# Kernel tuning notes

Measured on AMD Instinct MI355X. Metric: run time of the kernel, lower is better.

Reference implementation:

```python
import jax, jax.numpy as jnp
import numpy as np

B, C, D, L, H = 128, 1000, 300, 40, 100


def setup_inputs() -> dict:
    key = jax.random.key(0)
    ks = jax.random.split(key, 16)
    def rn(i, shape, sc=1.0):
        return (jax.random.normal(ks[i], shape, jnp.float32) * sc).astype(jnp.float32)
    return {
        "utt": rn(0, (B, L, D)),
        "sys_slots": rn(1, (B, D), 0.1),
        "conf_slots": rn(2, (B, D), 0.1),
        "conf_values": rn(3, (B, D), 0.1),
        "y_past_state": jax.random.uniform(ks[4], (B, C), jnp.float32),
        "slot_emb": rn(5, (C, D), 0.1),
        "value_emb": rn(6, (C, D), 0.1),
        "Wc": rn(7, (D, 2 * D), 0.05), "bc": jnp.zeros((D,), jnp.float32),
        "conv_w1": rn(8, (D, D, 1), 0.05), "conv_b1": jnp.zeros((D,), jnp.float32),
        "conv_w2": rn(9, (D, D, 2), 0.05), "conv_b2": jnp.zeros((D,), jnp.float32),
        "conv_w3": rn(10, (D, D, 3), 0.05), "conv_b3": jnp.zeros((D,), jnp.float32),
        "Wd": rn(11, (H, D), 0.05), "bd": jnp.zeros((H,), jnp.float32),
        "Wmr": rn(12, (H, D), 0.05), "bmr": jnp.zeros((H,), jnp.float32),
        "Wmc": rn(13, (H, D), 0.05), "bmc": jnp.zeros((H,), jnp.float32),
        "Wj": rn(14, (1, H), 0.05), "bj": jnp.zeros((1,), jnp.float32),
    }


def _conv_relu_pool(x_ncl, w, b):
    # x_ncl: [B, D, L]; w: [F, D, k] -> relu(conv) then global max-pool over time -> [B, F]
    y = jax.lax.conv_general_dilated(x_ncl, w, (1,), 'VALID',
                                     dimension_numbers=('NCH', 'OIH', 'NCH'))
    y = jax.nn.relu(y + b[None, :, None])
    return jnp.max(y, axis=2)


def _sig_linear(x, W, b):
    # Sequential(Sigmoid, Linear): Linear applied to sigmoid(x)
    return jax.nn.sigmoid(x) @ W.T + b


def reference(utt, sys_slots, conf_slots, conf_values, y_past_state,
              slot_emb, value_emb, Wc, bc,
              conv_w1, conv_b1, conv_w2, conv_b2, conv_w3, conv_b3,
              Wd, bd, Wmr, bmr, Wmc, bmc, Wj, bj):
    # CNN utterance encoder: sum of 3 conv branches (filter widths 1,2,3)
    x = jnp.transpose(utt, (0, 2, 1))  # [B, D, L]
    final_utt = (_conv_relu_pool(x, conv_w1, conv_b1)
                 + _conv_relu_pool(x, conv_w2, conv_b2)
                 + _conv_relu_pool(x, conv_w3, conv_b3))  # [B, D]

    # candidates_transform = sigmoid(Linear(cat(slot_emb, value_emb)))
    cand = jax.nn.sigmoid(jnp.concatenate([slot_emb, value_emb], axis=1) @ Wc.T + bc)  # [C, D]

    # fused version of the per-batch repeat/addcmul loop: [B, C, D]
    contrib = cand[None, :, :] * final_utt[:, None, :]

    y1 = _sig_linear(_sig_linear(contrib, Wd, bd), Wj, bj)  # [B, C, 1]

    # system-act request gate: ([C,D]@[D,B]) @ [B,D] -> [C, D]
    m_r = (slot_emb @ sys_slots.T) @ final_utt
    y2 = _sig_linear(_sig_linear(m_r, Wmr, bmr), Wj, bj)  # [C, 1]

    # system-act confirm gate
    m_c = ((slot_emb @ conf_slots.T) * (value_emb @ conf_values.T)) @ final_utt  # [C, D]
    y3 = _sig_linear(_sig_linear(m_c, Wmc, bmc), Wj, bj)  # [C, 1]

    y_presoftmax = y1 + y2[None, :, :] + y3[None, :, :]  # [B, C, 1]
    combine = 0.5
    return combine * y_presoftmax[..., 0] + (1.0 - combine) * y_past_state  # [B, C]
```

## Files before the change

kernel.cpp:

```cpp
#include <hip/hip_runtime.h>
#include <hip/hip_bf16.h>

#define OFF_SYST    0
#define OFF_CONFST  153600
#define OFF_CONFVT  307200
#define OFF_WMRT    460800
#define OFF_WMCT    580800
#define OFF_FU      700800
#define OFF_Y23     854400
#define OFF_BDP     858432
#define OFF_WJP     858880
#define OFF_BCP     859392
#define OFF_XBF     860672
#define OFF_WALLT   4137472
#define OFF_PBF     5366272
#define OFF_FUBF    25027072
#define OFF_CATSV   25108992
#define OFF_WCPK    26419712
#define OFF_CANDBF  26829312
#define OFF_WDFRAG  27484672

typedef short bf16x8_t __attribute__((ext_vector_type(8)));
typedef float f32x4_t  __attribute__((ext_vector_type(4)));

__device__ __forceinline__ float sigmoidf_fast(float x) {
    return __builtin_amdgcn_rcpf(1.0f + __expf(-x));
}
__device__ __forceinline__ unsigned short f2bf(float x) {
    unsigned int u = __float_as_uint(x);
    unsigned int r = (u + 0x7FFFu + ((u >> 16) & 1u)) >> 16;
    return (unsigned short)r;
}
__device__ __forceinline__ float bf2f(unsigned short h) {
    return __uint_as_float(((unsigned int)h) << 16);
}

__global__ void pack_kernel(const float* __restrict__ w1, const float* __restrict__ w2,
                            const float* __restrict__ w3, const float* __restrict__ Wc,
                            const float* __restrict__ Wd, const float* __restrict__ Wmr,
                            const float* __restrict__ Wmc, const float* __restrict__ sys,
                            const float* __restrict__ confs, const float* __restrict__ confv,
                            const float* __restrict__ bd, const float* __restrict__ Wj,
                            const float* __restrict__ bc, const float* __restrict__ slot,
                            const float* __restrict__ value,
                            unsigned short* __restrict__ WallTbf,
                            unsigned short* __restrict__ WdFrag,
                            float* __restrict__ bdPad, float* __restrict__ WjPad,
                            float* __restrict__ bcPad,
                            float* __restrict__ sysT, float* __restrict__ confsT,
                            float* __restrict__ confvT, float* __restrict__ WmrT,
                            float* __restrict__ WmcT,
                            unsigned short* __restrict__ catsv,
                            unsigned short* __restrict__ WcPk) {
    int idx = blockIdx.x * blockDim.x + threadIdx.x;
    if (idx < 614400) {
        int tap = idx / 102400;
        int rem = idx - tap * 102400;
        int f = rem / 320, k = rem % 320;
        float v = 0.0f;
        if (f < 300 && k < 300) {
            int fd = f * 300 + k;
            if (tap == 0)      v = w1[fd];
            else if (tap == 1) v = w2[fd * 2 + 0];
            else if (tap == 2) v = w2[fd * 2 + 1];
            else               v = w3[fd * 3 + (tap - 3)];
        }
        WallTbf[idx] = f2bf(v);
    } else if (idx < 650240) {
        int i = idx - 614400;
        int entry = i >> 3, e = i & 7;
        int kt = entry / 448;
        int r = entry - kt * 448;
        int ni = r >> 6, lane = r & 63;
        int j = ni * 16 + (lane & 15);
        int k = kt * 32 + (lane >> 4) * 8 + e;
        float v = (j < 100 && k < 300) ? Wd[j * 300 + k] : 0.0f;
        WdFrag[i] = f2bf(v);
    } else if (idx < 650352) {
        int j = idx - 650240;
        bdPad[j] = (j < 100) ? bd[j] : 0.0f;
    } else if (idx < 650464) {
        int j = idx - 650352;
        WjPad[j] = (j < 100) ? Wj[j] : 0.0f;
    } else if (idx < 650784) {
        int j = idx - 650464;
        bcPad[j] = (j < 300) ? bc[j] : 0.0f;
    } else if (idx < 765984) {
        int i = idx - 650784; int m = i / 38400; int r = i % 38400;
        int d = r / 128, b = r % 128;
        const float* src = (m == 0) ? sys : ((m == 1) ? confs : confv);
        float* dst = (m == 0) ? sysT : ((m == 1) ? confsT : confvT);
        dst[r] = src[b * 300 + d];
    } else if (idx < 795984) {
        int i = idx - 765984; int f = i / 100, j = i % 100;
        WmrT[i] = Wmr[j * 300 + f];
    } else if (idx < 825984) {
        int i = idx - 795984; int f = i / 100, j = i % 100;
        WmcT[i] = Wmc[j * 300 + f];
    } else if (idx < 1481344) {
        int i = idx - 825984;
        int c = i / 640, k = i % 640;
        float v = 0.0f;
        if (c < 1000) {
            if (k < 300)                   v = slot[c * 300 + k];
            else if (k >= 320 && k < 620)  v = value[c * 300 + (k - 320)];
        }
        catsv[i] = f2bf(v);
    } else if (idx < 1686144) {
        int i = idx - 1481344;
        int f = i / 640, k = i % 640;
        float v = 0.0f;
        if (f < 300) {
            if (k < 300)                   v = Wc[f * 600 + k];
            else if (k >= 320 && k < 620)  v = Wc[f * 600 + 300 + (k - 320)];
        }
        WcPk[i] = f2bf(v);
    }
}

__global__ void xcvt_kernel(const float* __restrict__ utt, unsigned short* __restrict__ Xbf) {
    int idx = blockIdx.x * blockDim.x + threadIdx.x;
    int m = idx / 320, k = idx % 320;
    float v = (k < 300) ? utt[m * 300 + k] : 0.0f;
    Xbf[idx] = f2bf(v);
}

__global__ __launch_bounds__(256, 2) void gemm1_kernel(const unsigned short* __restrict__ Xbf,
        const unsigned short* __restrict__ WallTbf, unsigned short* __restrict__ Pbf) {
    __shared__ __attribute__((aligned(16))) short As[128 * 40];
    __shared__ __attribute__((aligned(16))) short Bs[128 * 40];
    const int tid = threadIdx.x;
    const int m0 = blockIdx.x * 128;
    const int n0 = blockIdx.y * 128;
    const int lane = tid & 63;
    const int w = tid >> 6;
    const int wrow = w >> 1, wcol = w & 1;
    const int ln = lane & 15, lq = lane >> 4;

    f32x4_t acc[4][4];
    #pragma unroll
    for (int i = 0; i < 4; i++)
        #pragma unroll
        for (int j = 0; j < 4; j++) acc[i][j] = (f32x4_t){0.f, 0.f, 0.f, 0.f};

    for (int kk = 0; kk < 320; kk += 32) {
        #pragma unroll
        for (int i = tid; i < 512; i += 256) {
            int row = i >> 2, q = i & 3;
            *(uint4*)(&As[row * 40 + q * 8]) =
                *(const uint4*)(Xbf + (m0 + row) * 320 + kk + q * 8);
        }
        #pragma unroll
        for (int i = tid; i < 512; i += 256) {
            int row = i >> 2, q = i & 3;
            *(uint4*)(&Bs[row * 40 + q * 8]) =
                *(const uint4*)(WallTbf + (n0 + row) * 320 + kk + q * 8);
        }
        __syncthreads();
        bf16x8_t a[4], b[4];
        #pragma unroll
        for (int mi = 0; mi < 4; mi++)
            a[mi] = *(const bf16x8_t*)(&As[(wrow * 64 + mi * 16 + ln) * 40 + lq * 8]);
        #pragma unroll
        for (int ni = 0; ni < 4; ni++)
            b[ni] = *(const bf16x8_t*)(&Bs[(wcol * 64 + ni * 16 + ln) * 40 + lq * 8]);
        #pragma unroll
        for (int mi = 0; mi < 4; mi++)
            #pragma unroll
            for (int ni = 0; ni < 4; ni++)
                acc[mi][ni] = __builtin_amdgcn_mfma_f32_16x16x32_bf16(a[mi], b[ni], acc[mi][ni], 0, 0, 0);
        __syncthreads();
    }
    #pragma unroll
    for (int mi = 0; mi < 4; mi++) {
        #pragma unroll
        for (int ni = 0; ni < 4; ni++) {
            int col = n0 + wcol * 64 + ni * 16 + ln;
            #pragma unroll
            for (int reg = 0; reg < 4; reg++) {
                int row = m0 + wrow * 64 + mi * 16 + lq * 4 + reg;
                Pbf[row * 1920 + col] = f2bf(acc[mi][ni][reg]);
            }
        }
    }
}

__global__ __launch_bounds__(320) void combine_kernel(const unsigned short* __restrict__ Pbf,
        const float* __restrict__ b1, const float* __restrict__ b2,
        const float* __restrict__ b3, float* __restrict__ fu,
        unsigned short* __restrict__ fubf) {
    int b = blockIdx.x;
    int f = threadIdx.x;
    if (f >= 300) { fubf[b * 320 + f] = 0; return; }
    const unsigned short* base = Pbf + (size_t)b * 40 * 1920;
    float m1 = -1e30f, m2 = -1e30f, m3 = -1e30f;
    float p1prev = 0.f, p3prev = 0.f, p3prev2 = 0.f, p4prev = 0.f;
    for (int t = 0; t < 40; ++t) {
        const unsigned short* r = base + t * 1920;
        float p0 = bf2f(r[f]);
        float p1 = bf2f(r[320 + f]);
        float p2 = bf2f(r[640 + f]);
        float p3 = bf2f(r[960 + f]);
        float p4 = bf2f(r[1280 + f]);
        float p5 = bf2f(r[1600 + f]);
        m1 = fmaxf(m1, p0);
        if (t >= 1) m2 = fmaxf(m2, p1prev + p2);
        if (t >= 2) m3 = fmaxf(m3, p3prev2 + p4prev + p5);
        p3prev2 = p3prev; p3prev = p3; p4prev = p4; p1prev = p1;
    }
    float r = fmaxf(m1 + b1[f], 0.f) + fmaxf(m2 + b2[f], 0.f) + fmaxf(m3 + b3[f], 0.f);
    fu[b * 300 + f]   = r;
    fubf[b * 320 + f] = f2bf(r);
}

__global__ __launch_bounds__(256) void cand_gemm(const unsigned short* __restrict__ catsv,
        const unsigned short* __restrict__ WcPk, const float* __restrict__ bcPad,
        unsigned short* __restrict__ candbf) {
    __shared__ __attribute__((aligned(16))) short As[64 * 40];
    __shared__ __attribute__((aligned(16))) short Bs[64 * 40];
    const int tid = threadIdx.x;
    const int m0 = blockIdx.x * 64, n0 = blockIdx.y * 64;
    const int lane = tid & 63, w = tid >> 6;
    const int wr = w & 1, wc = w >> 1;
    const int ln = lane & 15, lq = lane >> 4;
    f32x4_t acc[2][2];
    #pragma unroll
    for (int i = 0; i < 2; i++)
        #pragma unroll
        for (int j = 0; j < 2; j++) acc[i][j] = (f32x4_t){0.f, 0.f, 0.f, 0.f};
    const int srow = tid >> 2, sq = tid & 3;
    for (int kk = 0; kk < 640; kk += 32) {
        *(uint4*)(&As[srow * 40 + sq * 8]) = *(const uint4*)(catsv + (m0 + srow) * 640 + kk + sq * 8);
        *(uint4*)(&Bs[srow * 40 + sq * 8]) = *(const uint4*)(WcPk  + (n0 + srow) * 640 + kk + sq * 8);
        __syncthreads();
        bf16x8_t a[2], b[2];
        #pragma unroll
        for (int mi = 0; mi < 2; mi++)
            a[mi] = *(const bf16x8_t*)(&As[(wr * 32 + mi * 16 + ln) * 40 + lq * 8]);
        #pragma unroll
        for (int ni = 0; ni < 2; ni++)
            b[ni] = *(const bf16x8_t*)(&Bs[(wc * 32 + ni * 16 + ln) * 40 + lq * 8]);
        #pragma unroll
        for (int mi = 0; mi < 2; mi++)
            #pragma unroll
            for (int ni = 0; ni < 2; ni++)
                acc[mi][ni] = __builtin_amdgcn_mfma_f32_16x16x32_bf16(a[mi], b[ni], acc[mi][ni], 0, 0, 0);
        __syncthreads();
    }
    #pragma unroll
    for (int mi = 0; mi < 2; mi++) {
        #pragma unroll
        for (int ni = 0; ni < 2; ni++) {
            int n = n0 + wc * 32 + ni * 16 + ln;
            float bcv = bcPad[n];
            #pragma unroll
            for (int reg = 0; reg < 4; reg++) {
                int cr = m0 + wr * 32 + mi * 16 + lq * 4 + reg;
                candbf[cr * 320 + n] = f2bf(sigmoidf_fast(acc[mi][ni][reg] + bcv));
            }
        }
    }
}

__global__ __launch_bounds__(128) void gates_kernel(const float* __restrict__ slot,
        const float* __restrict__ value, const float* __restrict__ sysT,
        const float* __restrict__ confsT, const float* __restrict__ confvT,
        const float* __restrict__ fu, const float* __restrict__ WmrT,
        const float* __restrict__ bmr, const float* __restrict__ WmcT,
        const float* __restrict__ bmc, const float* __restrict__ Wj,
        const float* __restrict__ bj, float* __restrict__ y23) {
    int c = blockIdx.x;
    int tid = threadIdx.x;
    __shared__ float spr[128], spc[128];
    __shared__ float smr[300], smc[300];
    __shared__ float red[128];
    {
        float pr = 0.f, ps = 0.f, pv = 0.f;
        const float* se = slot + c * 300;
        const float* ve = value + c * 300;
        for (int d = 0; d < 300; ++d) {
            float s = se[d], v = ve[d];
            pr += s * sysT[d * 128 + tid];
            ps += s * confsT[d * 128 + tid];
            pv += v * confvT[d * 128 + tid];
        }
        spr[tid] = pr;
        spc[tid] = ps * pv;
    }
    __syncthreads();
    for (int f = tid; f < 300; f += 128) {
        float mr = 0.f, mc = 0.f;
        for (int b = 0; b < 128; ++b) {
            float fv = fu[b * 300 + f];
            mr += spr[b] * fv;
            mc += spc[b] * fv;
        }
        smr[f] = sigmoidf_fast(mr);
        smc[f] = sigmoidf_fast(mc);
    }
    __syncthreads();
    float contrib = 0.f;
    if (tid < 100) {
        float hr = 0.f, hc = 0.f;
        for (int ff = 0; ff < 300; ++ff) {
            hr += smr[ff] * WmrT[ff * 100 + tid];
            hc += smc[ff] * WmcT[ff * 100 + tid];
        }
        hr = sigmoidf_fast(hr + bmr[tid]);
        hc = sigmoidf_fast(hc + bmc[tid]);
        contrib = (hr + hc) * Wj[tid];
    }
    red[tid] = contrib;
    __syncthreads();
    for (int s = 64; s > 0; s >>= 1) {
        if (tid < s) red[tid] += red[tid + s];
        __syncthreads();
    }
    if (tid == 0) y23[c] = red[0] + 2.0f * bj[0];
}

__global__ __launch_bounds__(256) void gemm2_kernel(const unsigned short* __restrict__ candbf,
        const unsigned short* __restrict__ fubf, const unsigned short* __restrict__ WdFrag,
        const float* __restrict__ bdPad, const float* __restrict__ WjPad,
        const float* __restrict__ bj, const float* __restrict__ y23,
        const float* __restrict__ ypast, float* __restrict__ out) {
    __shared__ __attribute__((aligned(16))) short Bs[2][3584];
    __shared__ float bdS[112], WjS[112], ybuf[128];
    const int c = blockIdx.x;
    const int tid = threadIdx.x;
    const int lane = tid & 63, w = tid >> 6;
    const int ln = lane & 15, lq = lane >> 4;
    if (tid < 112) { bdS[tid] = bdPad[tid]; WjS[tid] = WjPad[tid]; }

    const unsigned short* candRow = candbf + c * 320;
    const unsigned short* fuR0 = fubf + (w * 32 + ln) * 320;
    const unsigned short* fuR1 = fuR0 + 16 * 320;

    f32x4_t acc[2][7];
    #pragma unroll
    for (int mi = 0; mi < 2; mi++)
        #pragma unroll
        for (int ni = 0; ni < 7; ni++) acc[mi][ni] = (f32x4_t){0.f, 0.f, 0.f, 0.f};

    {
        const uint4* src = (const uint4*)(WdFrag);
        uint4* dst = (uint4*)&Bs[0][0];
        dst[tid] = src[tid];
        if (tid < 192) dst[tid + 256] = src[tid + 256];
    }
    __syncthreads();

    #pragma unroll
    for (int kt = 0; kt < 10; kt++) {
        if (kt < 9) {
            const uint4* src = (const uint4*)(WdFrag + (kt + 1) * 3584);
            uint4* dst = (uint4*)&Bs[(kt + 1) & 1][0];
            dst[tid] = src[tid];
            if (tid < 192) dst[tid + 256] = src[tid + 256];
        }
        const int k0 = kt * 32 + lq * 8;
        bf16x8_t cf  = *(const bf16x8_t*)(candRow + k0);
        bf16x8_t f0v = *(const bf16x8_t*)(fuR0 + k0);
        bf16x8_t f1v = *(const bf16x8_t*)(fuR1 + k0);
        bf16x8_t a0, a1;
        #pragma unroll
        for (int e = 0; e < 8; e += 2) {
            float cv0 = bf2f((unsigned short)cf[e]);
            float cv1 = bf2f((unsigned short)cf[e + 1]);
            float2 s0 = make_float2(sigmoidf_fast(cv0 * bf2f((unsigned short)f0v[e])),
                                    sigmoidf_fast(cv1 * bf2f((unsigned short)f0v[e + 1])));
            float2 s1 = make_float2(sigmoidf_fast(cv0 * bf2f((unsigned short)f1v[e])),
                                    sigmoidf_fast(cv1 * bf2f((unsigned short)f1v[e + 1])));
            __hip_bfloat162 p0 = __float22bfloat162_rn(s0);
            __hip_bfloat162 p1 = __float22bfloat162_rn(s1);
            ((unsigned int*)&a0)[e >> 1] = *(unsigned int*)&p0;
            ((unsigned int*)&a1)[e >> 1] = *(unsigned int*)&p1;
        }
        #pragma unroll
        for (int ni = 0; ni < 7; ni++) {
            bf16x8_t bfr = *(const bf16x8_t*)(&Bs[kt & 1][(ni * 64 + lane) * 8]);
            acc[0][ni] = __builtin_amdgcn_mfma_f32_16x16x32_bf16(a0, bfr, acc[0][ni], 0, 0, 0);
            acc[1][ni] = __builtin_amdgcn_mfma_f32_16x16x32_bf16(a1, bfr, acc[1][ni], 0, 0, 0);
        }
        __syncthreads();
    }

    float psum[2][4] = {{0.f, 0.f, 0.f, 0.f}, {0.f, 0.f, 0.f, 0.f}};
    #pragma unroll
    for (int mi = 0; mi < 2; mi++) {
        #pragma unroll
        for (int ni = 0; ni < 7; ni++) {
            int n = ni * 16 + ln;
            float bdv = bdS[n], wjv = WjS[n];
            #pragma unroll
            for (int reg = 0; reg < 4; reg++) {
                float h = sigmoidf_fast(acc[mi][ni][reg] + bdv);
                psum[mi][reg] += h * wjv;
            }
        }
    }
    #pragma unroll
    for (int mi = 0; mi < 2; mi++) {
        #pragma unroll
        for (int reg = 0; reg < 4; reg++) {
            float v = psum[mi][reg];
            v += __shfl_xor(v, 1);
            v += __shfl_xor(v, 2);
            v += __shfl_xor(v, 4);
            v += __shfl_xor(v, 8);
            if (ln == 0) ybuf[w * 32 + mi * 16 + lq * 4 + reg] = v;
        }
    }
    __syncthreads();
    if (tid < 128) {
        int b = tid;
        float y1 = ybuf[b] + bj[0];
        out[b * 1000 + c] = 0.5f * (y1 + y23[c]) + 0.5f * ypast[b * 1000 + c];
    }
}

extern "C" void kernel_launch(void* const* d_in, const int* in_sizes, int n_in,
                              void* d_out, int out_size, void* d_ws, size_t ws_size,
                              hipStream_t stream) {
    const float* utt   = (const float*)d_in[0];
    const float* sys   = (const float*)d_in[1];
    const float* confs = (const float*)d_in[2];
    const float* confv = (const float*)d_in[3];
    const float* ypast = (const float*)d_in[4];
    const float* slot  = (const float*)d_in[5];
    const float* value = (const float*)d_in[6];
    const float* Wc    = (const float*)d_in[7];
    const float* bc    = (const float*)d_in[8];
    const float* w1    = (const float*)d_in[9];
    const float* b1    = (const float*)d_in[10];
    const float* w2    = (const float*)d_in[11];
    const float* b2    = (const float*)d_in[12];
    const float* w3    = (const float*)d_in[13];
    const float* b3    = (const float*)d_in[14];
    const float* Wd    = (const float*)d_in[15];
    const float* bd    = (const float*)d_in[16];
    const float* Wmr   = (const float*)d_in[17];
    const float* bmr   = (const float*)d_in[18];
    const float* Wmc   = (const float*)d_in[19];
    const float* bmc   = (const float*)d_in[20];
    const float* Wj    = (const float*)d_in[21];
    const float* bj    = (const float*)d_in[22];

    char* wsb = (char*)d_ws;
    float* sysT   = (float*)(wsb + OFF_SYST);
    float* confsT = (float*)(wsb + OFF_CONFST);
    float* confvT = (float*)(wsb + OFF_CONFVT);
    float* WmrT   = (float*)(wsb + OFF_WMRT);
    float* WmcT   = (float*)(wsb + OFF_WMCT);
    float* fu     = (float*)(wsb + OFF_FU);
    float* y23    = (float*)(wsb + OFF_Y23);
    float* bdPad  = (float*)(wsb + OFF_BDP);
    float* WjPad  = (float*)(wsb + OFF_WJP);
    float* bcPad  = (float*)(wsb + OFF_BCP);
    unsigned short* Xbf     = (unsigned short*)(wsb + OFF_XBF);
    unsigned short* WallTbf = (unsigned short*)(wsb + OFF_WALLT);
    unsigned short* Pbf     = (unsigned short*)(wsb + OFF_PBF);
    unsigned short* fubf    = (unsigned short*)(wsb + OFF_FUBF);
    unsigned short* catsv   = (unsigned short*)(wsb + OFF_CATSV);
    unsigned short* WcPk    = (unsigned short*)(wsb + OFF_WCPK);
    unsigned short* candbf  = (unsigned short*)(wsb + OFF_CANDBF);
    unsigned short* WdFrag  = (unsigned short*)(wsb + OFF_WDFRAG);
    float* out = (float*)d_out;

    pack_kernel<<<6587, 256, 0, stream>>>(w1, w2, w3, Wc, Wd, Wmr, Wmc, sys, confs, confv,
                                          bd, Wj, bc, slot, value,
                                          WallTbf, WdFrag, bdPad, WjPad, bcPad,
                                          sysT, confsT, confvT, WmrT, WmcT, catsv, WcPk);
    xcvt_kernel<<<6400, 256, 0, stream>>>(utt, Xbf);
    gemm1_kernel<<<dim3(40, 15), 256, 0, stream>>>(Xbf, WallTbf, Pbf);
    combine_kernel<<<128, 320, 0, stream>>>(Pbf, b1, b2, b3, fu, fubf);
    cand_gemm<<<dim3(16, 5), 256, 0, stream>>>(catsv, WcPk, bcPad, candbf);
    gates_kernel<<<1000, 128, 0, stream>>>(slot, value, sysT, confsT, confvT, fu,
                                           WmrT, bmr, WmcT, bmc, Wj, bj, y23);
    gemm2_kernel<<<1000, 256, 0, stream>>>(candbf, fubf, WdFrag, bdPad, WjPad,
                                           bj, y23, ypast, out);
}
```

Measured before the change: 220.1 us.

## Replace scalar gates kernel with three bf16 MFMA GEMMs and fuse utt conversion

The per-slot scalar FP32 gates kernel, which computed three matvecs, then a 128-length reduction and a 300x100 projection for each of 1000 slots, is replaced by three MFMA GEMM kernels. pgate_gemm computes the slot/sys/conf projections, mgate_gemm multiplies them by the transposed bf16 final_utt, and ygate_gemm applies the Wmr/Wmc layers plus the Wj reduction. The separate utt-to-bf16 conversion kernel is removed, and gemm1 now converts fp32 utt directly while loading its tile into shared memory. This removes one launch and a large amount of scalar FMA work, but adds two launches and lowers gate precision to bf16. pgate_gemm and ygate_gemm run only 16 blocks each.

```diff
diff --git a/kernel.cpp b/kernel.cpp
--- a/kernel.cpp
+++ b/kernel.cpp
@@ -1,24 +1,29 @@
 #include <hip/hip_runtime.h>
 #include <hip/hip_bf16.h>
 
-#define OFF_SYST    0
-#define OFF_CONFST  153600
-#define OFF_CONFVT  307200
-#define OFF_WMRT    460800
-#define OFF_WMCT    580800
-#define OFF_FU      700800
-#define OFF_Y23     854400
-#define OFF_BDP     858432
-#define OFF_WJP     858880
-#define OFF_BCP     859392
-#define OFF_XBF     860672
-#define OFF_WALLT   4137472
-#define OFF_PBF     5366272
-#define OFF_FUBF    25027072
-#define OFF_CATSV   25108992
-#define OFF_WCPK    26419712
-#define OFF_CANDBF  26829312
-#define OFF_WDFRAG  27484672
+#define OFF_Y23     0
+#define OFF_BDP     4096
+#define OFF_WJP     4544
+#define OFF_BCP     4992
+#define OFF_BMRP    6272
+#define OFF_BMCP    6720
+#define OFF_WALLT   7168
+#define OFF_PBF     1235968
+#define OFF_FUBF    20896768
+#define OFF_FUBFT   20978688
+#define OFF_CATSV   21060608
+#define OFF_WCPK    22371328
+#define OFF_CANDBF  22780928
+#define OFF_WDFRAG  23436288
+#define OFF_WMRFRAG 23507968
+#define OFF_WMCFRAG 23579648
+#define OFF_SYSB    23651328
+#define OFF_CONFSB  23733248
+#define OFF_CONFVB  23815168
+#define OFF_PRBF    23897088
+#define OFF_PCBF    24159232
+#define OFF_SMRBF   24421376
+#define OFF_SMCBF   25076736
 
 typedef short bf16x8_t __attribute__((ext_vector_type(8)));
 typedef float f32x4_t  __attribute__((ext_vector_type(4)));
@@ -33,6 +38,16 @@
 }
 __device__ __forceinline__ float bf2f(unsigned short h) {
     return __uint_as_float(((unsigned int)h) << 16);
+}
+
+__device__ __forceinline__ float frag_fetch(const float* __restrict__ W, int i) {
+    int entry = i >> 3, e = i & 7;
+    int kt = entry / 448;
+    int r = entry - kt * 448;
+    int ni = r >> 6, lane = r & 63;
+    int j = ni * 16 + (lane & 15);
+    int k = kt * 32 + (lane >> 4) * 8 + e;
+    return (j < 100 && k < 300) ? W[j * 300 + k] : 0.0f;
 }
 
 __global__ void pack_kernel(const float* __restrict__ w1, const float* __restrict__ w2,
@@ -41,15 +56,19 @@
                             const float* __restrict__ Wmc, const float* __restrict__ sys,
                             const float* __restrict__ confs, const float* __restrict__ confv,
                             const float* __restrict__ bd, const float* __restrict__ Wj,
+                            const float* __restrict__ bmr, const float* __restrict__ bmc,
                             const float* __restrict__ bc, const float* __restrict__ slot,
                             const float* __restrict__ value,
                             unsigned short* __restrict__ WallTbf,
                             unsigned short* __restrict__ WdFrag,
+                            unsigned short* __restrict__ WmrFrag,
+                            unsigned short* __restrict__ WmcFrag,
                             float* __restrict__ bdPad, float* __restrict__ WjPad,
+                            float* __restrict__ bmrPad, float* __restrict__ bmcPad,
                             float* __restrict__ bcPad,
-                            float* __restrict__ sysT, float* __restrict__ confsT,
-                            float* __restrict__ confvT, float* __restrict__ WmrT,
-                            float* __restrict__ WmcT,
+                            unsigned short* __restrict__ sysB,
+                            unsigned short* __restrict__ confsB,
+                            unsigned short* __restrict__ confvB,
                             unsigned short* __restrict__ catsv,
                             unsigned short* __restrict__ WcPk) {
     int idx = blockIdx.x * blockDim.x + threadIdx.x;
@@ -68,37 +87,32 @@
         WallTbf[idx] = f2bf(v);
     } else if (idx < 650240) {
         int i = idx - 614400;
-        int entry = i >> 3, e = i & 7;
-        int kt = entry / 448;
-        int r = entry - kt * 448;
-        int ni = r >> 6, lane = r & 63;
-        int j = ni * 16 + (lane & 15);
-        int k = kt * 32 + (lane >> 4) * 8 + e;
-        float v = (j < 100 && k < 300) ? Wd[j * 300 + k] : 0.0f;
-        WdFrag[i] = f2bf(v);
-    } else if (idx < 650352) {
-        int j = idx - 650240;
-        bdPad[j] = (j < 100) ? bd[j] : 0.0f;
-    } else if (idx < 650464) {
-        int j = idx - 650352;
-        WjPad[j] = (j < 100) ? Wj[j] : 0.0f;
-    } else if (idx < 650784) {
-        int j = idx - 650464;
-        bcPad[j] = (j < 300) ? bc[j] : 0.0f;
-    } else if (idx < 765984) {
-        int i = idx - 650784; int m = i / 38400; int r = i % 38400;
-        int d = r / 128, b = r % 128;
+        WdFrag[i] = f2bf(frag_fetch(Wd, i));
+    } else if (idx < 686080) {
+        int i = idx - 650240;
+        WmrFrag[i] = f2bf(frag_fetch(Wmr, i));
+    } else if (idx < 721920) {
+        int i = idx - 686080;
+        WmcFrag[i] = f2bf(frag_fetch(Wmc, i));
+    } else if (idx < 722032) {
+        int j = idx - 721920; bdPad[j] = (j < 100) ? bd[j] : 0.0f;
+    } else if (idx < 722144) {
+        int j = idx - 722032; WjPad[j] = (j < 100) ? Wj[j] : 0.0f;
+    } else if (idx < 722256) {
+        int j = idx - 722144; bmrPad[j] = (j < 100) ? bmr[j] : 0.0f;
+    } else if (idx < 722368) {
+        int j = idx - 722256; bmcPad[j] = (j < 100) ? bmc[j] : 0.0f;
+    } else if (idx < 722688) {
+        int j = idx - 722368; bcPad[j] = (j < 300) ? bc[j] : 0.0f;
+    } else if (idx < 845568) {
+        int i = idx - 722688;
+        int m = i / 40960, r = i % 40960;
+        int b = r / 320, k = r % 320;
         const float* src = (m == 0) ? sys : ((m == 1) ? confs : confv);
-        float* dst = (m == 0) ? sysT : ((m == 1) ? confsT : confvT);
-        dst[r] = src[b * 300 + d];
-    } else if (idx < 795984) {
-        int i = idx - 765984; int f = i / 100, j = i % 100;
-        WmrT[i] = Wmr[j * 300 + f];
-    } else if (idx < 825984) {
-        int i = idx - 795984; int f = i / 100, j = i % 100;
-        WmcT[i] = Wmc[j * 300 + f];
-    } else if (idx < 1481344) {
-        int i = idx - 825984;
+        unsigned short* dst = (m == 0) ? sysB : ((m == 1) ? confsB : confvB);
+        dst[r] = f2bf((k < 300) ? src[b * 300 + k] : 0.0f);
+    } else if (idx < 1500928) {
+        int i = idx - 845568;
         int c = i / 640, k = i % 640;
         float v = 0.0f;
         if (c < 1000) {
@@ -106,8 +120,8 @@
             else if (k >= 320 && k < 620)  v = value[c * 300 + (k - 320)];
         }
         catsv[i] = f2bf(v);
-    } else if (idx < 1686144) {
-        int i = idx - 1481344;
+    } else if (idx < 1705728) {
+        int i = idx - 1500928;
         int f = i / 640, k = i % 640;
         float v = 0.0f;
         if (f < 300) {
@@ -118,14 +132,7 @@
     }
 }
 
-__global__ void xcvt_kernel(const float* __restrict__ utt, unsigned short* __restrict__ Xbf) {
-    int idx = blockIdx.x * blockDim.x + threadIdx.x;
-    int m = idx / 320, k = idx % 320;
-    float v = (k < 300) ? utt[m * 300 + k] : 0.0f;
-    Xbf[idx] = f2bf(v);
-}
-
-__global__ __launch_bounds__(256, 2) void gemm1_kernel(const unsigned short* __restrict__ Xbf,
+__global__ __launch_bounds__(256, 2) void gemm1_kernel(const float* __restrict__ utt,
         const unsigned short* __restrict__ WallTbf, unsigned short* __restrict__ Pbf) {
     __shared__ __attribute__((aligned(16))) short As[128 * 40];
     __shared__ __attribute__((aligned(16))) short Bs[128 * 40];
@@ -147,8 +154,24 @@
         #pragma unroll
         for (int i = tid; i < 512; i += 256) {
             int row = i >> 2, q = i & 3;
-            *(uint4*)(&As[row * 40 + q * 8]) =
-                *(const uint4*)(Xbf + (m0 + row) * 320 + kk + q * 8);
+            int k0 = kk + q * 8;
+            const float* src = utt + (m0 + row) * 300;
+            bf16x8_t v;
+            if (k0 + 8 <= 300) {
+                float4 f0 = *(const float4*)(src + k0);
+                float4 f1 = *(const float4*)(src + k0 + 4);
+                v[0] = (short)f2bf(f0.x); v[1] = (short)f2bf(f0.y);
+                v[2] = (short)f2bf(f0.z); v[3] = (short)f2bf(f0.w);
+                v[4] = (short)f2bf(f1.x); v[5] = (short)f2bf(f1.y);
+                v[6] = (short)f2bf(f1.z); v[7] = (short)f2bf(f1.w);
+            } else {
+                #pragma unroll
+                for (int e = 0; e < 8; e++) {
+                    int k = k0 + e;
+                    v[e] = (k < 300) ? (short)f2bf(src[k]) : (short)0;
+                }
+            }
+            *(bf16x8_t*)(&As[row * 40 + q * 8]) = v;
         }
         #pragma unroll
         for (int i = tid; i < 512; i += 256) {
@@ -187,11 +210,11 @@
 
 __global__ __launch_bounds__(320) void combine_kernel(const unsigned short* __restrict__ Pbf,
         const float* __restrict__ b1, const float* __restrict__ b2,
-        const float* __restrict__ b3, float* __restrict__ fu,
-        unsigned short* __restrict__ fubf) {
+        const float* __restrict__ b3, unsigned short* __restrict__ fubf,
+        unsigned short* __restrict__ fubfT) {
     int b = blockIdx.x;
     int f = threadIdx.x;
-    if (f >= 300) { fubf[b * 320 + f] = 0; return; }
+    if (f >= 300) { fubf[b * 320 + f] = 0; fubfT[f * 128 + b] = 0; return; }
     const unsigned short* base = Pbf + (size_t)b * 40 * 1920;
     float m1 = -1e30f, m2 = -1e30f, m3 = -1e30f;
     float p1prev = 0.f, p3prev = 0.f, p3prev2 = 0.f, p4prev = 0.f;
@@ -209,8 +232,9 @@
         p3prev2 = p3prev; p3prev = p3; p4prev = p4; p1prev = p1;
     }
     float r = fmaxf(m1 + b1[f], 0.f) + fmaxf(m2 + b2[f], 0.f) + fmaxf(m3 + b3[f], 0.f);
-    fu[b * 300 + f]   = r;
-    fubf[b * 320 + f] = f2bf(r);
+    unsigned short rb = f2bf(r);
+    fubf[b * 320 + f]  = rb;
+    fubfT[f * 128 + b] = rb;
 }
 
 __global__ __launch_bounds__(256) void cand_gemm(const unsigned short* __restrict__ catsv,
@@ -262,61 +286,200 @@
     }
 }
 
-__global__ __launch_bounds__(128) void gates_kernel(const float* __restrict__ slot,
-        const float* __restrict__ value, const float* __restrict__ sysT,
-        const float* __restrict__ confsT, const float* __restrict__ confvT,
-        const float* __restrict__ fu, const float* __restrict__ WmrT,
-        const float* __restrict__ bmr, const float* __restrict__ WmcT,
-        const float* __restrict__ bmc, const float* __restrict__ Wj,
+__global__ __launch_bounds__(256) void pgate_gemm(const unsigned short* __restrict__ catsv,
+        const unsigned short* __restrict__ sysB, const unsigned short* __restrict__ confsB,
+        const unsigned short* __restrict__ confvB,
+        unsigned short* __restrict__ Prbf, unsigned short* __restrict__ Pcbf) {
+    __shared__ __attribute__((aligned(16))) short As[2][64 * 40];
+    __shared__ __attribute__((aligned(16))) short Bs[3][128 * 40];
+    const int tid = threadIdx.x;
+    const int c0 = blockIdx.x * 64;
+    const int lane = tid & 63, w = tid >> 6;
+    const int ln = lane & 15, lq = lane >> 4;
+    f32x4_t accR[8], accS[8], accV[8];
+    #pragma unroll
+    for (int i = 0; i < 8; i++) {
+        accR[i] = (f32x4_t){0.f, 0.f, 0.f, 0.f};
+        accS[i] = (f32x4_t){0.f, 0.f, 0.f, 0.f};
+        accV[i] = (f32x4_t){0.f, 0.f, 0.f, 0.f};
+    }
+    for (int kk = 0; kk < 320; kk += 32) {
+        #pragma unroll
+        for (int i = tid; i < 512; i += 256) {
+            int mat = i >> 8, r2 = i & 255;
+            int row = r2 >> 2, q = r2 & 3;
+            *(uint4*)(&As[mat][row * 40 + q * 8]) =
+                *(const uint4*)(catsv + (c0 + row) * 640 + mat * 320 + kk + q * 8);
+        }
+        #pragma unroll
+        for (int i = tid; i < 1536; i += 256) {
+            int mat = i >> 9, r2 = i & 511;
+            int row = r2 >> 2, q = r2 & 3;
+            const unsigned short* src = (mat == 0) ? sysB : ((mat == 1) ? confsB : confvB);
+            *(uint4*)(&Bs[mat][row * 40 + q * 8]) =
+                *(const uint4*)(src + row * 320 + kk + q * 8);
+        }
+        __syncthreads();
+        bf16x8_t aS = *(const bf16x8_t*)(&As[0][(w * 16 + ln) * 40 + lq * 8]);
+        bf16x8_t aV = *(const bf16x8_t*)(&As[1][(w * 16 + ln) * 40 + lq * 8]);
+        #pragma unroll
+        for (int ni = 0; ni < 8; ni++) {
+            bf16x8_t bR = *(const bf16x8_t*)(&Bs[0][(ni * 16 + ln) * 40 + lq * 8]);
+            bf16x8_t bS = *(const bf16x8_t*)(&Bs[1][(ni * 16 + ln) * 40 + lq * 8]);
+            bf16x8_t bV = *(const bf16x8_t*)(&Bs[2][(ni * 16 + ln) * 40 + lq * 8]);
+            accR[ni] = __builtin_amdgcn_mfma_f32_16x16x32_bf16(aS, bR, accR[ni], 0, 0, 0);
+            accS[ni] = __builtin_amdgcn_mfma_f32_16x16x32_bf16(aS, bS, accS[ni], 0, 0, 0);
+            accV[ni] = __builtin_amdgcn_mfma_f32_16x16x32_bf16(aV, bV, accV[ni], 0, 0, 0);
+        }
+        __syncthreads();
+    }
+    #pragma unroll
+    for (int ni = 0; ni < 8; ni++) {
+        int b = ni * 16 + ln;
+        #pragma unroll
+        for (int reg = 0; reg < 4; reg++) {
+            int c = c0 + w * 16 + lq * 4 + reg;
+            Prbf[c * 128 + b] = f2bf(accR[ni][reg]);
+            Pcbf[c * 128 + b] = f2bf(accS[ni][reg] * accV[ni][reg]);
+        }
+    }
+}
+
+__global__ __launch_bounds__(256) void mgate_gemm(const unsigned short* __restrict__ Prbf,
+        const unsigned short* __restrict__ Pcbf, const unsigned short* __restrict__ fubfT,
+        unsigned short* __restrict__ smrbf, unsigned short* __restrict__ smcbf) {
+    __shared__ __attribute__((aligned(16))) short As[2][64 * 40];
+    __shared__ __attribute__((aligned(16))) short Bs[64 * 40];
+    const int tid = threadIdx.x;
+    const int m0 = blockIdx.x * 64, n0 = blockIdx.y * 64;
+    const int lane = tid & 63, w = tid >> 6;
+    const int wr = w & 1, wc = w >> 1;
+    const int ln = lane & 15, lq = lane >> 4;
+    f32x4_t accR[2][2], accC[2][2];
+    #pragma unroll
+    for (int i = 0; i < 2; i++)
+        #pragma unroll
+        for (int j = 0; j < 2; j++) {
+            accR[i][j] = (f32x4_t){0.f, 0.f, 0.f, 0.f};
+            accC[i][j] = (f32x4_t){0.f, 0.f, 0.f, 0.f};
+        }
+    for (int kk = 0; kk < 128; kk += 32) {
+        #pragma unroll
+        for (int i = tid; i < 512; i += 256) {
+            int mat = i >> 8, r2 = i & 255;
+            int row = r2 >> 2, q = r2 & 3;
+            const unsigned short* src = mat ? Pcbf : Prbf;
+            *(uint4*)(&As[mat][row * 40 + q * 8]) =
+                *(const uint4*)(src + (m0 + row) * 128 + kk + q * 8);
+        }
+        if (tid < 256) {
+            int row = tid >> 2, q = tid & 3;
+            *(uint4*)(&Bs[row * 40 + q * 8]) =
+                *(const uint4*)(fubfT + (n0 + row) * 128 + kk + q * 8);
+        }
+        __syncthreads();
+        bf16x8_t aR[2], aC[2], b[2];
+        #pragma unroll
+        for (int mi = 0; mi < 2; mi++) {
+            aR[mi] = *(const bf16x8_t*)(&As[0][(wr * 32 + mi * 16 + ln) * 40 + lq * 8]);
+            aC[mi] = *(const bf16x8_t*)(&As[1][(wr * 32 + mi * 16 + ln) * 40 + lq * 8]);
+        }
+        #pragma unroll
+        for (int ni = 0; ni < 2; ni++)
+            b[ni] = *(const bf16x8_t*)(&Bs[(wc * 32 + ni * 16 + ln) * 40 + lq * 8]);
+        #pragma unroll
+        for (int mi = 0; mi < 2; mi++)
+            #pragma unroll
+            for (int ni = 0; ni < 2; ni++) {
+                accR[mi][ni] = __builtin_amdgcn_mfma_f32_16x16x32_bf16(aR[mi], b[ni], accR[mi][ni], 0, 0, 0);
+                accC[mi][ni] = __builtin_amdgcn_mfma_f32_16x16x32_bf16(aC[mi], b[ni], accC[mi][ni], 0, 0, 0);
+            }
+        __syncthreads();
+    }
+    #pragma unroll
+    for (int mi = 0; mi < 2; mi++) {
+        #pragma unroll
+        for (int ni = 0; ni < 2; ni++) {
+            int f = n0 + wc * 32 + ni * 16 + ln;
+            #pragma unroll
+            for (int reg = 0; reg < 4; reg++) {
+                int c = m0 + wr * 32 + mi * 16 + lq * 4 + reg;
+                smrbf[c * 320 + f] = f2bf(sigmoidf_fast(accR[mi][ni][reg]));
+                smcbf[c * 320 + f] = f2bf(sigmoidf_fast(accC[mi][ni][reg]));
+            }
+        }
+    }
+}
+
+__global__ __launch_bounds__(256) void ygate_gemm(const unsigned short* __restrict__ smrbf,
+        const unsigned short* __restrict__ smcbf, const unsigned short* __restrict__ WmrFrag,
+        const unsigned short* __restrict__ WmcFrag, const float* __restrict__ bmrPad,
+        const float* __restrict__ bmcPad, const float* __restrict__ WjPad,
         const float* __restrict__ bj, float* __restrict__ y23) {
-    int c = blockIdx.x;
-    int tid = threadIdx.x;
-    __shared__ float spr[128], spc[128];
-    __shared__ float smr[300], smc[300];
-    __shared__ float red[128];
-    {
-        float pr = 0.f, ps = 0.f, pv = 0.f;
-        const float* se = slot + c * 300;
-        const float* ve = value + c * 300;
-        for (int d = 0; d < 300; ++d) {
-            float s = se[d], v = ve[d];
-            pr += s * sysT[d * 128 + tid];
-            ps += s * confsT[d * 128 + tid];
-            pv += v * confvT[d * 128 + tid];
-        }
-        spr[tid] = pr;
-        spc[tid] = ps * pv;
-    }
-    __syncthreads();
-    for (int f = tid; f < 300; f += 128) {
-        float mr = 0.f, mc = 0.f;
-        for (int b = 0; b < 128; ++b) {
-            float fv = fu[b * 300 + f];
-            mr += spr[b] * fv;
-            mc += spc[b] * fv;
-        }
-        smr[f] = sigmoidf_fast(mr);
-        smc[f] = sigmoidf_fast(mc);
-    }
-    __syncthreads();
-    float contrib = 0.f;
-    if (tid < 100) {
-        float hr = 0.f, hc = 0.f;
-        for (int ff = 0; ff < 300; ++ff) {
-            hr += smr[ff] * WmrT[ff * 100 + tid];
-            hc += smc[ff] * WmcT[ff * 100 + tid];
-        }
-        hr = sigmoidf_fast(hr + bmr[tid]);
-        hc = sigmoidf_fast(hc + bmc[tid]);
-        contrib = (hr + hc) * Wj[tid];
-    }
-    red[tid] = contrib;
-    __syncthreads();
-    for (int s = 64; s > 0; s >>= 1) {
-        if (tid < s) red[tid] += red[tid + s];
-        __syncthreads();
-    }
-    if (tid == 0) y23[c] = red[0] + 2.0f * bj[0];
+    __shared__ __attribute__((aligned(16))) short As[2][64 * 40];
+    __shared__ __attribute__((aligned(16))) short Bs[2][3584];
+    const int tid = threadIdx.x;
+    const int c0 = blockIdx.x * 64;
+    const int lane = tid & 63, w = tid >> 6;
+    const int ln = lane & 15, lq = lane >> 4;
+    f32x4_t accR[7], accC[7];
+    #pragma unroll
+    for (int i = 0; i < 7; i++) {
+        accR[i] = (f32x4_t){0.f, 0.f, 0.f, 0.f};
+        accC[i] = (f32x4_t){0.f, 0.f, 0.f, 0.f};
+    }
+    for (int kt = 0; kt < 10; kt++) {
+        int kk = kt * 32;
+        #pragma unroll
+        for (int i = tid; i < 512; i += 256) {
+            int mat = i >> 8, r2 = i & 255;
+            int row = r2 >> 2, q = r2 & 3;
+            const unsigned short* src = mat ? smcbf : smrbf;
+            *(uint4*)(&As[mat][row * 40 + q * 8]) =
+                *(const uint4*)(src + (c0 + row) * 320 + kk + q * 8);
+        }
+        #pragma unroll
+        for (int i = tid; i < 896; i += 256) {
+            int mat = i / 448, j = i - mat * 448;
+            const uint4* s = (const uint4*)((mat ? WmcFrag : WmrFrag) + kt * 3584);
+            ((uint4*)&Bs[mat][0])[j] = s[j];
+        }
+        __syncthreads();
+        bf16x8_t aR = *(const bf16x8_t*)(&As[0][(w * 16 + ln) * 40 + lq * 8]);
+        bf16x8_t aC = *(const bf16x8_t*)(&As[1][(w * 16 + ln) * 40 + lq * 8]);
+        #pragma unroll
+        for (int ni = 0; ni < 7; ni++) {
+            bf16x8_t bR = *(const bf16x8_t*)(&Bs[0][(ni * 64 + lane) * 8]);
+            bf16x8_t bC = *(const bf16x8_t*)(&Bs[1][(ni * 64 + lane) * 8]);
+            accR[ni] = __builtin_amdgcn_mfma_f32_16x16x32_bf16(aR, bR, accR[ni], 0, 0, 0);
+            accC[ni] = __builtin_amdgcn_mfma_f32_16x16x32_bf16(aC, bC, accC[ni], 0, 0, 0);
+        }
+        __syncthreads();
+    }
+    float psum[4] = {0.f, 0.f, 0.f, 0.f};
+    #pragma unroll
+    for (int ni = 0; ni < 7; ni++) {
+        int n = ni * 16 + ln;
+        float wj = WjPad[n], br = bmrPad[n], bcv = bmcPad[n];
+        #pragma unroll
+        for (int reg = 0; reg < 4; reg++) {
+            float hr = sigmoidf_fast(accR[ni][reg] + br);
+            float hc = sigmoidf_fast(accC[ni][reg] + bcv);
+            psum[reg] += (hr + hc) * wj;
+        }
+    }
+    #pragma unroll
+    for (int reg = 0; reg < 4; reg++) {
+        float v = psum[reg];
+        v += __shfl_xor(v, 1);
+        v += __shfl_xor(v, 2);
+        v += __shfl_xor(v, 4);
+        v += __shfl_xor(v, 8);
+        if (ln == 0) {
+            int c = c0 + w * 16 + lq * 4 + reg;
+            y23[c] = v + 2.0f * bj[0];
+        }
+    }
 }
 
 __global__ __launch_bounds__(256) void gemm2_kernel(const unsigned short* __restrict__ candbf,
@@ -447,36 +610,45 @@
     const float* bj    = (const float*)d_in[22];
 
     char* wsb = (char*)d_ws;
-    float* sysT   = (float*)(wsb + OFF_SYST);
-    float* confsT = (float*)(wsb + OFF_CONFST);
-    float* confvT = (float*)(wsb + OFF_CONFVT);
-    float* WmrT   = (float*)(wsb + OFF_WMRT);
-    float* WmcT   = (float*)(wsb + OFF_WMCT);
-    float* fu     = (float*)(wsb + OFF_FU);
     float* y23    = (float*)(wsb + OFF_Y23);
     float* bdPad  = (float*)(wsb + OFF_BDP);
     float* WjPad  = (float*)(wsb + OFF_WJP);
     float* bcPad  = (float*)(wsb + OFF_BCP);
-    unsigned short* Xbf     = (unsigned short*)(wsb + OFF_XBF);
+    float* bmrPad = (float*)(wsb + OFF_BMRP);
+    float* bmcPad = (float*)(wsb + OFF_BMCP);
     unsigned short* WallTbf = (unsigned short*)(wsb + OFF_WALLT);
     unsigned short* Pbf     = (unsigned short*)(wsb + OFF_PBF);
     unsigned short* fubf    = (unsigned short*)(wsb + OFF_FUBF);
+    unsigned short* fubfT   = (unsigned short*)(wsb + OFF_FUBFT);
     unsigned short* catsv   = (unsigned short*)(wsb + OFF_CATSV);
     unsigned short* WcPk    = (unsigned short*)(wsb + OFF_WCPK);
     unsigned short* candbf  = (unsigned short*)(wsb + OFF_CANDBF);
     unsigned short* WdFrag  = (unsigned short*)(wsb + OFF_WDFRAG);
+    unsigned short* WmrFrag = (unsigned short*)(wsb + OFF_WMRFRAG);
+    unsigned short* WmcFrag = (unsigned short*)(wsb + OFF_WMCFRAG);
+    unsigned short* sysB    = (unsigned short*)(wsb + OFF_SYSB);
+    unsigned short* confsB  = (unsigned short*)(wsb + OFF_CONFSB);
+    unsigned short* confvB  = (unsigned short*)(wsb + OFF_CONFVB);
     float* out = (float*)d_out;
 
-    pack_kernel<<<6587, 256, 0, stream>>>(w1, w2, w3, Wc, Wd, Wmr, Wmc, sys, confs, confv,
-                                          bd, Wj, bc, slot, value,
-                                          WallTbf, WdFrag, bdPad, WjPad, bcPad,
-                                          sysT, confsT, confvT, WmrT, WmcT, catsv, WcPk);
-    xcvt_kernel<<<6400, 256, 0, stream>>>(utt, Xbf);
-    gemm1_kernel<<<dim3(40, 15), 256, 0, stream>>>(Xbf, WallTbf, Pbf);
-    combine_kernel<<<128, 320, 0, stream>>>(Pbf, b1, b2, b3, fu, fubf);
+    pack_kernel<<<6663, 256, 0, stream>>>(w1, w2, w3, Wc, Wd, Wmr, Wmc, sys, confs, confv,
+                                          bd, Wj, bmr, bmc, bc, slot, value,
+                                          WallTbf, WdFrag, WmrFrag, WmcFrag,
+                                          bdPad, WjPad, bmrPad, bmcPad, bcPad,
+                                          sysB, confsB, confvB, catsv, WcPk);
+    gemm1_kernel<<<dim3(40, 15), 256, 0, stream>>>(utt, WallTbf, Pbf);
+    combine_kernel<<<128, 320, 0, stream>>>(Pbf, b1, b2, b3, fubf, fubfT);
     cand_gemm<<<dim3(16, 5), 256, 0, stream>>>(catsv, WcPk, bcPad, candbf);
-    gates_kernel<<<1000, 128, 0, stream>>>(slot, value, sysT, confsT, confvT, fu,
-                                           WmrT, bmr, WmcT, bmc, Wj, bj, y23);
+    pgate_gemm<<<16, 256, 0, stream>>>(catsv, sysB, confsB, confvB,
+                                       (unsigned short*)(wsb + OFF_PRBF),
+                                       (unsigned short*)(wsb + OFF_PCBF));
+    mgate_gemm<<<dim3(16, 5), 256, 0, stream>>>((unsigned short*)(wsb + OFF_PRBF),
+                                                (unsigned short*)(wsb + OFF_PCBF), fubfT,
+                                                (unsigned short*)(wsb + OFF_SMRBF),
+                                                (unsigned short*)(wsb + OFF_SMCBF));
+    ygate_gemm<<<16, 256, 0, stream>>>((unsigned short*)(wsb + OFF_SMRBF),
+                                       (unsigned short*)(wsb + OFF_SMCBF),
+                                       WmrFrag, WmcFrag, bmrPad, bmcPad, WjPad, bj, y23);
     gemm2_kernel<<<1000, 256, 0, stream>>>(candbf, fubf, WdFrag, bdPad, WjPad,
                                            bj, y23, ypast, out);
 }
```

Measured after the change: 220.7 us. No clear change (+0.3%).
